# Kernel tuning notes

Hardware: AMD Instinct MI355X
Metric: run time of the kernel (lower is better)

The kernel has to match this reference:

```python
import jax, jax.numpy as jnp
import numpy as np

# Static problem dims (match input_specs / init_kwargs)
B, NQ, C, H = 2, 900, 256, 8
HGT, WID = 64, 64            # single-scale feature map (input_spatial_shapes = [[64, 64]])
N = HGT * WID                # 4096 keys
DH = C // H                  # head dim 32
RPE_HID = 512
STRIDE = 16                  # feature_stride


def setup_inputs() -> dict:
    key = jax.random.key(0)
    ks = jax.random.split(key, 24)
    p = lambda k, shape: jax.random.normal(k, shape, jnp.float32) * 0.02
    # reference boxes (cx, cy, w, h) in pixel coords of a 1024x1024 image
    ref = jax.random.uniform(ks[0], (B, NQ, 1, 4), jnp.float32)
    ref = jnp.concatenate([ref[..., :2] * (WID * STRIDE), ref[..., 2:] * 128.0], axis=-1)
    return {
        "vggt_features": jnp.zeros((1,), jnp.float32),  # unused by forward (kept for signature fidelity)
        "query": jax.random.normal(ks[1], (B, NQ, C), jnp.float32),
        "reference_2d": ref,
        "k_input_flatten": jax.random.normal(ks[2], (B, N, C), jnp.float32),
        "v_input_flatten": jax.random.normal(ks[3], (B, N, C), jnp.float32),
        "input_spatial_shapes": jnp.array([[HGT, WID]], jnp.int32),
        "input_padding_mask": jnp.zeros((B, N), jnp.bool_),
        # cpb_mlp1 (x) and cpb_mlp2 (y): Linear(2,512)+ReLU+Linear(512,H,no bias); stored as [in,out]
        "W1x": p(ks[4], (2, RPE_HID)), "b1x": jnp.zeros((RPE_HID,), jnp.float32), "W2x": p(ks[5], (RPE_HID, H)),
        "W1y": p(ks[6], (2, RPE_HID)), "b1y": jnp.zeros((RPE_HID,), jnp.float32), "W2y": p(ks[7], (RPE_HID, H)),
        "Wq": p(ks[8], (C, C)), "bq": jnp.zeros((C,), jnp.float32),
        "Wk": p(ks[9], (C, C)), "bk": jnp.zeros((C,), jnp.float32),
        "Wv": p(ks[10], (C, C)), "bv": jnp.zeros((C,), jnp.float32),
        "Wp": p(ks[11], (C, C)), "bp": jnp.zeros((C,), jnp.float32),
    }


def _mlp(d, W1, b1, W2):
    return jax.nn.relu(d @ W1 + b1) @ W2


def reference(vggt_features, query, reference_2d, k_input_flatten, v_input_flatten,
              input_spatial_shapes, input_padding_mask,
              W1x, b1x, W2x, W1y, b1y, W2y, Wq, bq, Wk, bk, Wv, bv, Wp, bp):
    h, w = HGT, WID  # static (input_spatial_shapes[0] == [HGT, WID])
    scale = DH ** -0.5
    # cxcywh -> xyxy: [B, NQ, 1, 4]
    xyxy = jnp.concatenate([reference_2d[..., :2] - reference_2d[..., 2:] / 2,
                            reference_2d[..., :2] + reference_2d[..., 2:] / 2], axis=-1)
    # pixel-center grid coords (linspace(0.5, w-0.5, w) * stride)
    pos_x = ((jnp.arange(w, dtype=jnp.float32) + 0.5) * STRIDE)[None, None, :, None]
    pos_y = ((jnp.arange(h, dtype=jnp.float32) + 0.5) * STRIDE)[None, None, :, None]
    delta_x = xyxy[..., 0::2] - pos_x  # [B, NQ, w, 2]  (x1, x2 rel. to columns)
    delta_y = xyxy[..., 1::2] - pos_y  # [B, NQ, h, 2]  (y1, y2 rel. to rows)
    rpe_x = _mlp(delta_x, W1x, b1x, W2x)  # [B, NQ, w, H]
    rpe_y = _mlp(delta_y, W1y, b1y, W2y)  # [B, NQ, h, H]
    # broadcast add over (row, col) then flatten spatial -> [B, H, NQ, N]
    rpe = (rpe_x[:, :, None] + rpe_y[:, :, :, None]).reshape(B, NQ, h * w, H).transpose(0, 3, 1, 2)
    q = (query @ Wq + bq).reshape(B, NQ, H, DH).transpose(0, 2, 1, 3) * scale  # [B,H,NQ,DH]
    k = (k_input_flatten @ Wk + bk).reshape(B, N, H, DH).transpose(0, 2, 1, 3)  # [B,H,N,DH]
    v = (v_input_flatten @ Wv + bv).reshape(B, N, H, DH).transpose(0, 2, 1, 3)  # [B,H,N,DH]
    attn = jnp.einsum('bhqd,bhkd->bhqk', q, k) + rpe
    attn = attn + input_padding_mask[:, None, None, :].astype(attn.dtype) * (-100.0)
    # torch.clip_ to finfo(min,max) is an identity on finite values; softmax follows
    attn = jax.nn.softmax(attn, axis=-1)
    x = jnp.einsum('bhqk,bhkd->bhqd', attn, v).transpose(0, 2, 1, 3).reshape(B, NQ, C)
    return x @ Wp + bp
```

## Files before the change

### kernel.cpp

```cpp
#include <hip/hip_runtime.h>
#include <hip/hip_bf16.h>
#include <cmath>

#define B_ 2
#define NQ_ 900
#define N_ 4096
#define LOG2E 1.4426950408889634f

typedef __attribute__((ext_vector_type(4))) float f32x4;
typedef __attribute__((ext_vector_type(8))) short s16x8;
typedef __attribute__((ext_vector_type(8))) _Float16 f16x8;

__device__ inline short f2bf(float x) {
    union { __hip_bfloat16 b; short s; } u;
    u.b = __float2bfloat16(x);
    return u.s;
}
__device__ inline short f2h(float x) {
    _Float16 h = (_Float16)x;
    return __builtin_bit_cast(short, h);
}

template <int CTRL>
__device__ inline float dppf(float x) {
    int xi = __builtin_bit_cast(int, x);
    int r = __builtin_amdgcn_update_dpp(xi, xi, CTRL, 0xF, 0xF, true);
    return __builtin_bit_cast(float, r);
}
__device__ inline float rowmax16(float v) {
    v = fmaxf(v, dppf<0x121>(v));
    v = fmaxf(v, dppf<0x122>(v));
    v = fmaxf(v, dppf<0x124>(v));
    v = fmaxf(v, dppf<0x128>(v));
    return v;
}
__device__ inline float rowsum16(float v) {
    v += dppf<0x121>(v);
    v += dppf<0x122>(v);
    v += dppf<0x124>(v);
    v += dppf<0x128>(v);
    return v;
}

__global__ __launch_bounds__(256) void proj_kernel(
    const float* __restrict__ query, const float* __restrict__ kin,
    const float* __restrict__ vin,
    const float* __restrict__ Wq, const float* __restrict__ Wk,
    const float* __restrict__ Wv,
    const float* __restrict__ bqv, const float* __restrict__ bkv,
    const float* __restrict__ bvv,
    unsigned short* __restrict__ qbf, unsigned short* __restrict__ kbf,
    unsigned short* __restrict__ vbf, float qscale)
{
    const int mtx = blockIdx.z;
    const float* X = mtx == 0 ? query : mtx == 1 ? kin : vin;
    const float* W = mtx == 0 ? Wq : mtx == 1 ? Wk : Wv;
    const float* bias = mtx == 0 ? bqv : mtx == 1 ? bkv : bvv;
    unsigned short* Y = mtx == 0 ? qbf : mtx == 1 ? kbf : vbf;
    const int M = mtx == 0 ? 1800 : 8192;
    const int m0 = blockIdx.x * 64;
    if (m0 >= M) return;
    const float alpha = mtx == 0 ? qscale : 1.0f;
    const int rows_per_b = mtx == 0 ? 900 : 4096;
    const int ROWS = mtx == 0 ? 960 : 4096;

    __shared__ short Ab[16384];
    __shared__ short Bb[16384];
    const int tid = threadIdx.x;
    const int w = tid >> 6, l = tid & 63, quad = l >> 4, l15 = l & 15;
    const int wq = tid & 3, mm = tid >> 2;

    {
        const bool valid = (m0 + mm) < M;
        const float* xr = X + (size_t)(m0 + mm) * 256;
        #pragma unroll
        for (int it = 0; it < 8; ++it) {
            int g2 = it * 4 + wq;
            float4 a0 = make_float4(0.f, 0.f, 0.f, 0.f), a1 = a0;
            if (valid) {
                a0 = *(const float4*)(xr + g2 * 8);
                a1 = *(const float4*)(xr + g2 * 8 + 4);
            }
            uint4 pk;
            pk.x = (unsigned)(unsigned short)f2bf(a0.x) | ((unsigned)(unsigned short)f2bf(a0.y) << 16);
            pk.y = (unsigned)(unsigned short)f2bf(a0.z) | ((unsigned)(unsigned short)f2bf(a0.w) << 16);
            pk.z = (unsigned)(unsigned short)f2bf(a1.x) | ((unsigned)(unsigned short)f2bf(a1.y) << 16);
            pk.w = (unsigned)(unsigned short)f2bf(a1.z) | ((unsigned)(unsigned short)f2bf(a1.w) << 16);
            *(uint4*)(Ab + (it * 256 + mm * 4 + wq) * 8) = pk;
        }
    }

    for (int nt0 = 0; nt0 < 4; ++nt0) {
        const int n0 = nt0 * 64;
        {
            const float* wcol = W + n0 + mm;
            #pragma unroll
            for (int it = 0; it < 8; ++it) {
                int g2 = it * 4 + wq;
                uint4 wk4;
                wk4.x = (unsigned)(unsigned short)f2bf(wcol[(g2 * 8 + 0) * 256])
                      | ((unsigned)(unsigned short)f2bf(wcol[(g2 * 8 + 1) * 256]) << 16);
                wk4.y = (unsigned)(unsigned short)f2bf(wcol[(g2 * 8 + 2) * 256])
                      | ((unsigned)(unsigned short)f2bf(wcol[(g2 * 8 + 3) * 256]) << 16);
                wk4.z = (unsigned)(unsigned short)f2bf(wcol[(g2 * 8 + 4) * 256])
                      | ((unsigned)(unsigned short)f2bf(wcol[(g2 * 8 + 5) * 256]) << 16);
                wk4.w = (unsigned)(unsigned short)f2bf(wcol[(g2 * 8 + 6) * 256])
                      | ((unsigned)(unsigned short)f2bf(wcol[(g2 * 8 + 7) * 256]) << 16);
                *(uint4*)(Bb + (it * 256 + mm * 4 + wq) * 8) = wk4;
            }
        }
        __syncthreads();

        f32x4 acc[4] = {{0.f,0.f,0.f,0.f},{0.f,0.f,0.f,0.f},{0.f,0.f,0.f,0.f},{0.f,0.f,0.f,0.f}};
        #pragma unroll
        for (int kc = 0; kc < 8; ++kc) {
            s16x8 a = *(const s16x8*)(Ab + (kc * 256 + (w * 16 + l15) * 4 + quad) * 8);
            #pragma unroll
            for (int nt = 0; nt < 4; ++nt) {
                s16x8 bf = *(const s16x8*)(Bb + (kc * 256 + (nt * 16 + l15) * 4 + quad) * 8);
                acc[nt] = __builtin_amdgcn_mfma_f32_16x16x32_bf16(a, bf, acc[nt], 0, 0, 0);
            }
        }
        __syncthreads();

        #pragma unroll
        for (int nt = 0; nt < 4; ++nt) {
            int n = n0 + nt * 16 + l15;
            float bs = bias[n];
            int h = n >> 5, d = n & 31;
            #pragma unroll
            for (int r = 0; r < 4; ++r) {
                int row = m0 + w * 16 + quad * 4 + r;
                if (row < M) {
                    int b = row / rows_per_b;
                    int pos = row - b * rows_per_b;
                    Y[((size_t)(b * 8 + h) * ROWS + pos) * 32 + d] =
                        (unsigned short)f2bf((acc[nt][r] + bs) * alpha);
                }
            }
        }
    }
}

__global__ __launch_bounds__(256) void outproj_kernel(
    const float* __restrict__ X, const float* __restrict__ W,
    const float* __restrict__ bias, float* __restrict__ Y, int M)
{
    __shared__ short Abh[4096], Abl[4096], Bbh[4096], Bbl[4096];
    const int tid = threadIdx.x;
    const int m0 = blockIdx.x * 64, n0 = blockIdx.y * 64;
    const int w = tid >> 6, l = tid & 63, quad = l >> 4, l15 = l & 15;
    const int wq = tid & 3, mm = tid >> 2;
    const bool valid = (m0 + mm) < M;
    const float* xr = X + (size_t)(m0 + mm) * 256;
    const float* wcol = W + n0 + mm;

    f32x4 acc[4] = {{0.f,0.f,0.f,0.f},{0.f,0.f,0.f,0.f},{0.f,0.f,0.f,0.f},{0.f,0.f,0.f,0.f}};

    for (int kq = 0; kq < 4; ++kq) {
        #pragma unroll
        for (int it = 0; it < 2; ++it) {
            int g2 = it * 4 + wq;
            int kbase = kq * 64 + g2 * 8;
            float av[8], bv[8];
            #pragma unroll
            for (int j = 0; j < 8; ++j) {
                av[j] = valid ? xr[kbase + j] : 0.f;
                bv[j] = wcol[(kbase + j) * 256];
            }
            uint4 ah, al, bh, bl;
            unsigned* ahp = (unsigned*)&ah; unsigned* alp = (unsigned*)&al;
            unsigned* bhp = (unsigned*)&bh; unsigned* blp = (unsigned*)&bl;
            #pragma unroll
            for (int j2 = 0; j2 < 4; ++j2) {
                _Float16 h0 = (_Float16)av[j2 * 2], h1 = (_Float16)av[j2 * 2 + 1];
                ahp[j2] = (unsigned)(unsigned short)__builtin_bit_cast(short, h0)
                        | ((unsigned)(unsigned short)__builtin_bit_cast(short, h1) << 16);
                alp[j2] = (unsigned)(unsigned short)f2h(av[j2 * 2] - (float)h0)
                        | ((unsigned)(unsigned short)f2h(av[j2 * 2 + 1] - (float)h1) << 16);
                _Float16 g0 = (_Float16)bv[j2 * 2], g1 = (_Float16)bv[j2 * 2 + 1];
                bhp[j2] = (unsigned)(unsigned short)__builtin_bit_cast(short, g0)
                        | ((unsigned)(unsigned short)__builtin_bit_cast(short, g1) << 16);
                blp[j2] = (unsigned)(unsigned short)f2h(bv[j2 * 2] - (float)g0)
                        | ((unsigned)(unsigned short)f2h(bv[j2 * 2 + 1] - (float)g1) << 16);
            }
            int gi = (it * 256 + mm * 4 + wq) * 8;
            *(uint4*)(Abh + gi) = ah;
            *(uint4*)(Abl + gi) = al;
            *(uint4*)(Bbh + gi) = bh;
            *(uint4*)(Bbl + gi) = bl;
        }
        __syncthreads();

        #pragma unroll
        for (int kc = 0; kc < 2; ++kc) {
            int ga = (kc * 256 + (w * 16 + l15) * 4 + quad) * 8;
            f16x8 ah = *(const f16x8*)(Abh + ga);
            f16x8 al = *(const f16x8*)(Abl + ga);
            #pragma unroll
            for (int nt = 0; nt < 4; ++nt) {
                int gb = (kc * 256 + (nt * 16 + l15) * 4 + quad) * 8;
                f16x8 bh = *(const f16x8*)(Bbh + gb);
                f16x8 bl = *(const f16x8*)(Bbl + gb);
                acc[nt] = __builtin_amdgcn_mfma_f32_16x16x32_f16(ah, bh, acc[nt], 0, 0, 0);
                acc[nt] = __builtin_amdgcn_mfma_f32_16x16x32_f16(ah, bl, acc[nt], 0, 0, 0);
                acc[nt] = __builtin_amdgcn_mfma_f32_16x16x32_f16(al, bh, acc[nt], 0, 0, 0);
            }
        }
        __syncthreads();
    }

    #pragma unroll
    for (int nt = 0; nt < 4; ++nt) {
        int n = n0 + nt * 16 + l15;
        float bs = bias[n];
        #pragma unroll
        for (int r = 0; r < 4; ++r) {
            int row = m0 + w * 16 + quad * 4 + r;
            if (row < M)
                Y[(size_t)row * 256 + n] = acc[nt][r] + bs;
        }
    }
}

__global__ __launch_bounds__(512) void rpe3_kernel(
    const float* __restrict__ ref2d,
    const float* __restrict__ W1x, const float* __restrict__ b1x,
    const float* __restrict__ W1y, const float* __restrict__ b1y,
    const float* __restrict__ W2x, const float* __restrict__ W2y,
    float* __restrict__ rpe_x, float* __restrict__ rpe_y)
{
    __shared__ short sw2h[8192], sw2l[8192];
    __shared__ float4 sW1p[576];
    __shared__ float2 sB1p[576];

    const int tid = threadIdx.x;
    for (int i = tid; i < 8192; i += 512) {
        int g = i >> 3, j = i & 7;
        int kcg = g >> 6, rr = g & 63, n = rr >> 2, q4 = rr & 3;
        int k = kcg * 32 + q4 * 8 + j;
        float val = ((n < 8) ? W2x[k * 8 + n] : W2y[k * 8 + (n - 8)]) * LOG2E;
        _Float16 hi = (_Float16)val;
        sw2h[i] = __builtin_bit_cast(short, hi);
        sw2l[i] = f2h(val - (float)hi);
    }
    if (tid < 512) {
        int i = tid;
        sW1p[(i >> 3) * 9 + (i & 7)] = make_float4(W1x[i], W1x[512 + i], W1y[i], W1y[512 + i]);
        sB1p[(i >> 3) * 9 + (i & 7)] = make_float2(b1x[i], b1y[i]);
    }

    const int w = tid >> 6, l = tid & 63, quad = l >> 4, l15 = l & 15;
    const int qi = w >> 2, wrow = w & 3;
    const int bq = blockIdx.x * 2 + qi;
    const float4 box = *(const float4*)(ref2d + (size_t)bq * 4);
    const int row = wrow * 16 + l15;
    const float pc = (row + 0.5f) * 16.0f;
    const float dx0 = (box.x - box.z * 0.5f) - pc;
    const float dx1 = (box.x + box.z * 0.5f) - pc;
    const float dy0 = (box.y - box.w * 0.5f) - pc;
    const float dy1 = (box.y + box.w * 0.5f) - pc;

    __syncthreads();

    f32x4 accx = {0.f, 0.f, 0.f, 0.f}, accy = {0.f, 0.f, 0.f, 0.f};
    for (int kc = 0; kc < 16; ++kc) {
        f16x8 axh, axl, ayh, ayl;
        #pragma unroll
        for (int i = 0; i < 8; ++i) {
            int gi = (kc * 4 + quad) * 9 + i;
            float4 w1 = sW1p[gi];
            float2 bb = sB1p[gi];
            float hx = fmaxf(fmaf(dx0, w1.x, fmaf(dx1, w1.y, bb.x)), 0.f);
            float hy = fmaxf(fmaf(dy0, w1.z, fmaf(dy1, w1.w, bb.y)), 0.f);
            _Float16 xh = (_Float16)hx;
            _Float16 yh = (_Float16)hy;
            axh[i] = xh;
            axl[i] = (_Float16)(hx - (float)xh);
            ayh[i] = yh;
            ayl[i] = (_Float16)(hy - (float)yh);
        }
        f16x8 bh = *(const f16x8*)(sw2h + (kc * 64 + l15 * 4 + quad) * 8);
        f16x8 bl = *(const f16x8*)(sw2l + (kc * 64 + l15 * 4 + quad) * 8);
        accx = __builtin_amdgcn_mfma_f32_16x16x32_f16(axh, bh, accx, 0, 0, 0);
        accx = __builtin_amdgcn_mfma_f32_16x16x32_f16(axh, bl, accx, 0, 0, 0);
        accx = __builtin_amdgcn_mfma_f32_16x16x32_f16(axl, bh, accx, 0, 0, 0);
        accy = __builtin_amdgcn_mfma_f32_16x16x32_f16(ayh, bh, accy, 0, 0, 0);
        accy = __builtin_amdgcn_mfma_f32_16x16x32_f16(ayh, bl, accy, 0, 0, 0);
        accy = __builtin_amdgcn_mfma_f32_16x16x32_f16(ayl, bh, accy, 0, 0, 0);
    }

    #pragma unroll
    for (int rr = 0; rr < 4; ++rr) {
        int row_out = wrow * 16 + quad * 4 + rr;
        size_t base = ((size_t)bq * 64 + row_out) * 8;
        if (l15 < 8) rpe_x[base + l15] = accx[rr];
        else         rpe_y[base + (l15 - 8)] = accy[rr];
    }
}

__global__ __launch_bounds__(512, 4) void attn_mfma_kernel(
    const unsigned short* __restrict__ qb16, const unsigned short* __restrict__ kb16,
    const unsigned short* __restrict__ vb16,
    const float* __restrict__ rpe_x, const float* __restrict__ rpe_y,
    const unsigned char* __restrict__ mask, float* __restrict__ xout)
{
    __shared__ short skf[4 * 2048];
    __shared__ short svt[4 * 2048];
    __shared__ short spb[8 * 544];
    __shared__ float ry[32 * 65];
    __shared__ unsigned long long smaskb[64];
    __shared__ float sm[8][16], sl[8][16], sLf[32];

    const int tid = threadIdx.x;
    const int qb = blockIdx.x, h = blockIdx.y, b = blockIdx.z;
    const int q0 = qb * 32;
    const int w = tid >> 6, l = tid & 63;
    const int qsub = w >> 2, g = w & 3;
    const int quad = l >> 4, l15 = l & 15;

    const unsigned short* qg = qb16 + (size_t)(b * 8 + h) * 960 * 32;
    const unsigned short* kg = kb16 + (size_t)(b * 8 + h) * 4096 * 32;
    const unsigned short* vg = vb16 + (size_t)(b * 8 + h) * 4096 * 32;

    for (int i = tid; i < 2048; i += 512) {
        int qq = q0 + (i >> 6), pos = i & 63;
        float vy = 0.f;
        if (qq < NQ_)
            vy = rpe_y[((size_t)(b * NQ_ + qq) * 64 + pos) * 8 + h];
        ry[(i >> 6) * 65 + pos] = vy;
    }
    #pragma unroll
    for (int j = 0; j < 8; ++j) {
        int c = w * 8 + j;
        unsigned long long bits = __ballot(mask[(size_t)b * N_ + c * 64 + l] != 0);
        if (l == 0) smaskb[c] = bits;
    }

    s16x8 qa = *(const s16x8*)(qg + (size_t)(q0 + qsub * 16 + l15) * 32 + quad * 8);

    f32x4 rx4[4];
    #pragma unroll
    for (int t = 0; t < 4; ++t)
        #pragma unroll
        for (int r = 0; r < 4; ++r) {
            int qq = q0 + qsub * 16 + quad * 4 + r;
            rx4[t][r] = (qq < NQ_)
                ? rpe_x[((size_t)(b * NQ_ + qq) * 64 + t * 16 + l15) * 8 + h] : 0.f;
        }

    const int sg = tid >> 7, role = (tid >> 6) & 1, stl = tid & 63;
    int eoff[4];
    if (role == 0) {
        #pragma unroll
        for (int t = 0; t < 4; ++t)
            eoff[t] = (t * 16 + (stl & 15)) * 32 + (stl >> 4) * 8;
    } else {
        #pragma unroll
        for (int t = 0; t < 4; ++t)
            eoff[t] = stl * 32 + t * 8;
    }
    const unsigned short* src = role ? vg : kg;

    uint4 pf[4];
    {
        size_t cb = (size_t)(sg * 16) * 2048;
        #pragma unroll
        for (int t = 0; t < 4; ++t) pf[t] = *(const uint4*)(src + cb + eoff[t]);
    }

    float mrow[4] = {-INFINITY, -INFINITY, -INFINITY, -INFINITY};
    float lrow[4] = {0.f, 0.f, 0.f, 0.f};
    f32x4 acc0 = {0.f, 0.f, 0.f, 0.f}, acc1 = {0.f, 0.f, 0.f, 0.f};
    short* pw = spb + w * 544;

    for (int i = 0; i < 16; ++i) {
        __syncthreads();
        if (role == 0) {
            #pragma unroll
            for (int t = 0; t < 4; ++t)
                *(uint4*)(skf + sg * 2048 + (t * 64 + stl) * 8) = pf[t];
        } else {
            short* vtw = svt + sg * 2048;
            #pragma unroll
            for (int t = 0; t < 4; ++t) {
                const unsigned short* pv = (const unsigned short*)&pf[t];
                #pragma unroll
                for (int j = 0; j < 8; ++j) {
                    int d = t * 8 + j;
                    vtw[d * 64 + (((stl >> 3) ^ (d & 7)) << 3) + (stl & 7)] = (short)pv[j];
                }
            }
        }
        __syncthreads();

        {
            int inext = (i + 1 < 16) ? i + 1 : 15;
            size_t cb = (size_t)(sg * 16 + inext) * 2048;
            #pragma unroll
            for (int t = 0; t < 4; ++t) pf[t] = *(const uint4*)(src + cb + eoff[t]);
        }

        const int cgc = g * 16 + i;
        const short* kf = skf + g * 2048;

        f32x4 sc[4];
        #pragma unroll
        for (int t = 0; t < 4; ++t) {
            s16x8 kb = *(const s16x8*)(kf + (t * 64 + l) * 8);
            sc[t] = __builtin_amdgcn_mfma_f32_16x16x32_bf16(qa, kb, rx4[t], 0, 0, 0);
        }
        float ryv[4];
        #pragma unroll
        for (int r = 0; r < 4; ++r)
            ryv[r] = ry[(qsub * 16 + quad * 4 + r) * 65 + cgc];
        unsigned long long mb = smaskb[cgc];
        if (mb) {
            #pragma unroll
            for (int t = 0; t < 4; ++t) {
                float mk = ((mb >> (t * 16 + l15)) & 1ULL) ? -144.2695f : 0.f;
                #pragma unroll
                for (int r = 0; r < 4; ++r) sc[t][r] += mk;
            }
        }
        #pragma unroll
        for (int t = 0; t < 4; ++t)
            #pragma unroll
            for (int r = 0; r < 4; ++r)
                sc[t][r] += ryv[r];

        float cm[4];
        #pragma unroll
        for (int r = 0; r < 4; ++r) {
            cm[r] = fmaxf(fmaxf(sc[0][r], sc[1][r]), fmaxf(sc[2][r], sc[3][r]));
            cm[r] = rowmax16(cm[r]);
        }
        float al[4];
        #pragma unroll
        for (int r = 0; r < 4; ++r) {
            float mnew = fmaxf(mrow[r], cm[r]);
            al[r] = exp2f(mrow[r] - mnew);
            mrow[r] = mnew;
            lrow[r] *= al[r];
            acc0[r] *= al[r];
            acc1[r] *= al[r];
        }
        #pragma unroll
        for (int t = 0; t < 4; ++t)
            #pragma unroll
            for (int r = 0; r < 4; ++r)
                sc[t][r] = exp2f(sc[t][r] - mrow[r]);
        #pragma unroll
        for (int r = 0; r < 4; ++r) {
            float rs = (sc[0][r] + sc[1][r]) + (sc[2][r] + sc[3][r]);
            lrow[r] += rowsum16(rs);
        }

        const short* vt = svt + g * 2048;
        #pragma unroll
        for (int hh = 0; hh < 2; ++hh) {
            #pragma unroll
            for (int tt = 0; tt < 2; ++tt) {
                int t = hh * 2 + tt;
                int gphys = (tt * 2 + (l15 >> 3)) ^ quad;
                #pragma unroll
                for (int r = 0; r < 4; ++r)
                    pw[(gphys * 17 + quad * 4 + r) * 8 + (l15 & 7)] = f2bf(sc[t][r]);
            }
            int gph_r = quad ^ (l15 >> 2);
            s16x8 pa  = *(const s16x8*)(pw + (gph_r * 17 + l15) * 8);
            int ksw = ((hh * 4 + quad) ^ (l15 & 7)) * 8;
            s16x8 vb0 = *(const s16x8*)(vt + l15 * 64 + ksw);
            s16x8 vb1 = *(const s16x8*)(vt + (16 + l15) * 64 + ksw);
            acc0 = __builtin_amdgcn_mfma_f32_16x16x32_bf16(pa, vb0, acc0, 0, 0, 0);
            acc1 = __builtin_amdgcn_mfma_f32_16x16x32_bf16(pa, vb1, acc1, 0, 0, 0);
        }
    }

    __syncthreads();
    if (l15 == 0) {
        #pragma unroll
        for (int r = 0; r < 4; ++r) {
            sm[w][quad * 4 + r] = mrow[r];
            sl[w][quad * 4 + r] = lrow[r];
        }
    }
    __syncthreads();
    float wgt[4], L4[4];
    #pragma unroll
    for (int r = 0; r < 4; ++r) {
        int qrow = quad * 4 + r;
        float mm = -INFINITY;
        #pragma unroll
        for (int gg = 0; gg < 4; ++gg) mm = fmaxf(mm, sm[qsub * 4 + gg][qrow]);
        float LL = 0.f;
        #pragma unroll
        for (int gg = 0; gg < 4; ++gg)
            LL += exp2f(sm[qsub * 4 + gg][qrow] - mm) * sl[qsub * 4 + gg][qrow];
        wgt[r] = exp2f(mrow[r] - mm);
        L4[r] = LL;
    }
    if (g == 0 && l15 == 0) {
        #pragma unroll
        for (int r = 0; r < 4; ++r) sLf[qsub * 16 + quad * 4 + r] = L4[r];
    }

    float* obuf = (float*)skf;
    for (int gg = 0; gg < 4; ++gg) {
        if (g == gg) {
            #pragma unroll
            for (int r = 0; r < 4; ++r) {
                int idx = (qsub * 16 + quad * 4 + r) * 33 + l15;
                float v0 = wgt[r] * acc0[r];
                float v1 = wgt[r] * acc1[r];
                if (gg == 0) { obuf[idx] = v0; obuf[idx + 16] = v1; }
                else         { obuf[idx] += v0; obuf[idx + 16] += v1; }
            }
        }
        __syncthreads();
    }

    for (int i = tid; i < 1024; i += 512) {
        int ql = i >> 5, d = i & 31;
        int qq = q0 + ql;
        if (qq < NQ_)
            xout[(size_t)(b * NQ_ + qq) * 256 + h * 32 + d] = obuf[ql * 33 + d] / sLf[ql];
    }
}

extern "C" void kernel_launch(void* const* d_in, const int* in_sizes, int n_in,
                              void* d_out, int out_size, void* d_ws, size_t ws_size,
                              hipStream_t stream)
{
    const float* query = (const float*)d_in[1];
    const float* ref2d = (const float*)d_in[2];
    const float* kin   = (const float*)d_in[3];
    const float* vin   = (const float*)d_in[4];
    const unsigned char* mask = (const unsigned char*)d_in[6];
    const float* W1x = (const float*)d_in[7];
    const float* b1x = (const float*)d_in[8];
    const float* W2x = (const float*)d_in[9];
    const float* W1y = (const float*)d_in[10];
    const float* b1y = (const float*)d_in[11];
    const float* W2y = (const float*)d_in[12];
    const float* Wq  = (const float*)d_in[13];
    const float* bq  = (const float*)d_in[14];
    const float* Wk  = (const float*)d_in[15];
    const float* bk  = (const float*)d_in[16];
    const float* Wv  = (const float*)d_in[17];
    const float* bv  = (const float*)d_in[18];
    const float* Wp  = (const float*)d_in[19];
    const float* bp  = (const float*)d_in[20];

    char* wsb = (char*)d_ws;
    unsigned short* qbf = (unsigned short*)(wsb);
    unsigned short* kbf = (unsigned short*)(wsb +   983040);
    unsigned short* vbf = (unsigned short*)(wsb +  5177344);
    float* rxws = (float*)(wsb +  9371648);
    float* ryws = (float*)(wsb + 13058048);
    float* xws  = (float*)(wsb + 16744448);
    float* out  = (float*)d_out;

    const float qscale = LOG2E / sqrtf(32.0f);

    proj_kernel<<<dim3(128, 1, 3), 256, 0, stream>>>(
        query, kin, vin, Wq, Wk, Wv, bq, bk, bv, qbf, kbf, vbf, qscale);
    rpe3_kernel<<<900, 512, 0, stream>>>(
        ref2d, W1x, b1x, W1y, b1y, W2x, W2y, rxws, ryws);
    attn_mfma_kernel<<<dim3(29, 8, B_), 512, 0, stream>>>(
        qbf, kbf, vbf, rxws, ryws, mask, xws);
    outproj_kernel<<<dim3(29, 4), 256, 0, stream>>>(xws, Wp, bp, out, 1800);
}
```

Measured before the change: 245.1 us.

## Lazy softmax rescale, deferred row sums, and head-major RPE layout

```diff
diff --git a/kernel.cpp b/kernel.cpp
--- a/kernel.cpp
+++ b/kernel.cpp
@@ -231,8 +231,7 @@
     float* __restrict__ rpe_x, float* __restrict__ rpe_y)
 {
     __shared__ short sw2h[8192], sw2l[8192];
-    __shared__ float4 sW1p[576];
-    __shared__ float2 sB1p[576];
+    __shared__ float4 sUV[2 * 576];
 
     const int tid = threadIdx.x;
     for (int i = tid; i < 8192; i += 512) {
@@ -244,22 +243,26 @@
         sw2h[i] = __builtin_bit_cast(short, hi);
         sw2l[i] = f2h(val - (float)hi);
     }
-    if (tid < 512) {
-        int i = tid;
-        sW1p[(i >> 3) * 9 + (i & 7)] = make_float4(W1x[i], W1x[512 + i], W1y[i], W1y[512 + i]);
-        sB1p[(i >> 3) * 9 + (i & 7)] = make_float2(b1x[i], b1y[i]);
+    {
+        int k = tid;
+        float w1x0 = W1x[k], w1x1 = W1x[512 + k];
+        float w1y0 = W1y[k], w1y1 = W1y[512 + k];
+        float bx = b1x[k], by = b1y[k];
+        float vx = -(w1x0 + w1x1), vy = -(w1y0 + w1y1);
+        #pragma unroll
+        for (int q2 = 0; q2 < 2; ++q2) {
+            const float4 bb = *(const float4*)(ref2d + (size_t)(blockIdx.x * 2 + q2) * 4);
+            float ux = fmaf(w1x0, bb.x - bb.z * 0.5f, fmaf(w1x1, bb.x + bb.z * 0.5f, bx));
+            float uy = fmaf(w1y0, bb.y - bb.w * 0.5f, fmaf(w1y1, bb.y + bb.w * 0.5f, by));
+            sUV[q2 * 576 + (k >> 3) * 9 + (k & 7)] = make_float4(ux, vx, uy, vy);
+        }
     }
 
     const int w = tid >> 6, l = tid & 63, quad = l >> 4, l15 = l & 15;
     const int qi = w >> 2, wrow = w & 3;
     const int bq = blockIdx.x * 2 + qi;
-    const float4 box = *(const float4*)(ref2d + (size_t)bq * 4);
     const int row = wrow * 16 + l15;
     const float pc = (row + 0.5f) * 16.0f;
-    const float dx0 = (box.x - box.z * 0.5f) - pc;
-    const float dx1 = (box.x + box.z * 0.5f) - pc;
-    const float dy0 = (box.y - box.w * 0.5f) - pc;
-    const float dy1 = (box.y + box.w * 0.5f) - pc;
 
     __syncthreads();
 
@@ -268,11 +271,9 @@
         f16x8 axh, axl, ayh, ayl;
         #pragma unroll
         for (int i = 0; i < 8; ++i) {
-            int gi = (kc * 4 + quad) * 9 + i;
-            float4 w1 = sW1p[gi];
-            float2 bb = sB1p[gi];
-            float hx = fmaxf(fmaf(dx0, w1.x, fmaf(dx1, w1.y, bb.x)), 0.f);
-            float hy = fmaxf(fmaf(dy0, w1.z, fmaf(dy1, w1.w, bb.y)), 0.f);
+            float4 u = sUV[qi * 576 + (kc * 4 + quad) * 9 + i];
+            float hx = fmaxf(fmaf(u.y, pc, u.x), 0.f);
+            float hy = fmaxf(fmaf(u.w, pc, u.z), 0.f);
             _Float16 xh = (_Float16)hx;
             _Float16 yh = (_Float16)hy;
             axh[i] = xh;
@@ -293,9 +294,8 @@
     #pragma unroll
     for (int rr = 0; rr < 4; ++rr) {
         int row_out = wrow * 16 + quad * 4 + rr;
-        size_t base = ((size_t)bq * 64 + row_out) * 8;
-        if (l15 < 8) rpe_x[base + l15] = accx[rr];
-        else         rpe_y[base + (l15 - 8)] = accy[rr];
+        if (l15 < 8) rpe_x[((size_t)l15 * 1800 + bq) * 64 + row_out] = accx[rr];
+        else         rpe_y[((size_t)(l15 - 8) * 1800 + bq) * 64 + row_out] = accy[rr];
     }
 }
 
@@ -322,12 +322,14 @@
     const unsigned short* qg = qb16 + (size_t)(b * 8 + h) * 960 * 32;
     const unsigned short* kg = kb16 + (size_t)(b * 8 + h) * 4096 * 32;
     const unsigned short* vg = vb16 + (size_t)(b * 8 + h) * 4096 * 32;
+    const float* rxh = rpe_x + ((size_t)h * 1800 + b * NQ_) * 64;
+    const float* ryh = rpe_y + ((size_t)h * 1800 + b * NQ_) * 64;
 
     for (int i = tid; i < 2048; i += 512) {
         int qq = q0 + (i >> 6), pos = i & 63;
         float vy = 0.f;
         if (qq < NQ_)
-            vy = rpe_y[((size_t)(b * NQ_ + qq) * 64 + pos) * 8 + h];
+            vy = ryh[(size_t)qq * 64 + pos];
         ry[(i >> 6) * 65 + pos] = vy;
     }
     #pragma unroll
@@ -345,8 +347,7 @@
         #pragma unroll
         for (int r = 0; r < 4; ++r) {
             int qq = q0 + qsub * 16 + quad * 4 + r;
-            rx4[t][r] = (qq < NQ_)
-                ? rpe_x[((size_t)(b * NQ_ + qq) * 64 + t * 16 + l15) * 8 + h] : 0.f;
+            rx4[t][r] = (qq < NQ_) ? rxh[(size_t)qq * 64 + t * 16 + l15] : 0.f;
         }
 
     const int sg = tid >> 7, role = (tid >> 6) & 1, stl = tid & 63;
@@ -423,38 +424,38 @@
                 for (int r = 0; r < 4; ++r) sc[t][r] += mk;
             }
         }
+
+        float cmr[4];
+        #pragma unroll
+        for (int r = 0; r < 4; ++r)
+            cmr[r] = fmaxf(fmaxf(sc[0][r], sc[1][r]), fmaxf(sc[2][r], sc[3][r])) + ryv[r];
+
+        int ok = (cmr[0] <= mrow[0] + 8.f) & (cmr[1] <= mrow[1] + 8.f)
+               & (cmr[2] <= mrow[2] + 8.f) & (cmr[3] <= mrow[3] + 8.f);
+        if (!__all(ok)) {
+            #pragma unroll
+            for (int r = 0; r < 4; ++r) {
+                float cm = rowmax16(cmr[r]);
+                float mnew = fmaxf(mrow[r], cm);
+                float al = exp2f(mrow[r] - mnew);
+                mrow[r] = mnew;
+                lrow[r] *= al;
+                acc0[r] *= al;
+                acc1[r] *= al;
+            }
+        }
+
+        float msub[4];
+        #pragma unroll
+        for (int r = 0; r < 4; ++r) msub[r] = mrow[r] - ryv[r];
         #pragma unroll
         for (int t = 0; t < 4; ++t)
             #pragma unroll
             for (int r = 0; r < 4; ++r)
-                sc[t][r] += ryv[r];
-
-        float cm[4];
-        #pragma unroll
-        for (int r = 0; r < 4; ++r) {
-            cm[r] = fmaxf(fmaxf(sc[0][r], sc[1][r]), fmaxf(sc[2][r], sc[3][r]));
-            cm[r] = rowmax16(cm[r]);
-        }
-        float al[4];
-        #pragma unroll
-        for (int r = 0; r < 4; ++r) {
-            float mnew = fmaxf(mrow[r], cm[r]);
-            al[r] = exp2f(mrow[r] - mnew);
-            mrow[r] = mnew;
-            lrow[r] *= al[r];
-            acc0[r] *= al[r];
-            acc1[r] *= al[r];
-        }
-        #pragma unroll
-        for (int t = 0; t < 4; ++t)
-            #pragma unroll
-            for (int r = 0; r < 4; ++r)
-                sc[t][r] = exp2f(sc[t][r] - mrow[r]);
-        #pragma unroll
-        for (int r = 0; r < 4; ++r) {
-            float rs = (sc[0][r] + sc[1][r]) + (sc[2][r] + sc[3][r]);
-            lrow[r] += rowsum16(rs);
-        }
+                sc[t][r] = exp2f(sc[t][r] - msub[r]);
+        #pragma unroll
+        for (int r = 0; r < 4; ++r)
+            lrow[r] += (sc[0][r] + sc[1][r]) + (sc[2][r] + sc[3][r]);
 
         const short* vt = svt + g * 2048;
         #pragma unroll
@@ -476,6 +477,9 @@
             acc1 = __builtin_amdgcn_mfma_f32_16x16x32_bf16(pa, vb1, acc1, 0, 0, 0);
         }
     }
+
+    #pragma unroll
+    for (int r = 0; r < 4; ++r) lrow[r] = rowsum16(lrow[r]);
 
     __syncthreads();
     if (l15 == 0) {
```

Measured after the change: 232.6 us (median of 2 runs). -5.1%, faster.
